# Kernel tuning notes

Measured on AMD Instinct MI355X. Metric: run time of the kernel, lower is better.

The kernel has to match this reference:

```python
import jax, jax.numpy as jnp
import numpy as np

N_NODES = 100000
BN_EPS = 1e-5


def gcn_conv(x, src, dst, W, b, n):
    # PyG GCNConv: add self-loops, symmetric norm D^-1/2 (A+I) D^-1/2, then linear.
    h = x @ W                                   # [N, F_out]
    deg = jnp.zeros((n,), h.dtype).at[dst].add(1.0)   # in-degree incl. self-loops
    dinv = jnp.where(deg > 0, jax.lax.rsqrt(deg), 0.0)
    norm = dinv[src] * dinv[dst]                # [E+N]
    msg = h[src] * norm[:, None]                # gather + scale, [E+N, F_out]
    out = jax.ops.segment_sum(msg, dst, num_segments=n)
    return out + b


def setup_inputs() -> dict:
    key = jax.random.key(0)
    ks = jax.random.split(key, 6)
    N, E, F_in, H, C = N_NODES, 1600000, 128, 64, 64
    x = jax.random.normal(ks[0], (N, F_in), dtype=jnp.float32)
    edge_index = jax.random.randint(ks[1], (2, E), 0, N, dtype=jnp.int64)
    W1 = jax.random.normal(ks[2], (F_in, H), dtype=jnp.float32) * (1.0 / np.sqrt(F_in))
    b1 = jnp.zeros((H,), jnp.float32)
    W2 = jax.random.normal(ks[3], (H, C), dtype=jnp.float32) * (1.0 / np.sqrt(H))
    b2 = jnp.zeros((C,), jnp.float32)
    gamma = jnp.ones((H,), jnp.float32)
    beta = jnp.zeros((H,), jnp.float32)
    return {"x": x, "edge_index": edge_index, "W1": W1, "b1": b1,
            "W2": W2, "b2": b2, "gamma": gamma, "beta": beta}


def reference(x, edge_index, W1, b1, W2, b2, gamma, beta):
    n = x.shape[0]
    loop = jnp.arange(n, dtype=edge_index.dtype)
    src = jnp.concatenate([edge_index[0], loop])
    dst = jnp.concatenate([edge_index[1], loop])
    # dropout(p=0.8) acts as identity in eval mode (deterministic baseline)
    h = gcn_conv(x, src, dst, W1, b1, n)
    # BatchNorm1d with batch statistics (biased var), as in training-mode math
    mean = jnp.mean(h, axis=0)
    var = jnp.mean(jnp.square(h - mean), axis=0)
    h = (h - mean) * jax.lax.rsqrt(var + BN_EPS) * gamma + beta
    h = jax.nn.relu(h)
    out = gcn_conv(h, src, dst, W2, b2, n)
    return out
```

## Files before the change

kernel.cpp:

```cpp
#include <hip/hip_runtime.h>

#define BN_EPS 1e-5f
#define SCAN_CHUNK 2048
#define EPB 16384
#define NBUCK 512
#define NBG 512

__device__ __forceinline__ float bf2f(unsigned short u) {
  return __uint_as_float(((unsigned)u) << 16);
}
__device__ __forceinline__ unsigned short f2bf(float f) {
  unsigned b = __float_as_uint(f);
  b += 0x7FFFu + ((b >> 16) & 1u);
  return (unsigned short)(b >> 16);
}

template<int K, bool FUSE_BN, bool SCALE>
__device__ __forceinline__ void gemm_persist(
    float* __restrict__ Ws, float* __restrict__ Xs, float* __restrict__ bn_s,
    int tile0, int stride, int nT,
    const float* __restrict__ X, const float* __restrict__ W,
    const float* __restrict__ dinv, const float* __restrict__ stats,
    const float* __restrict__ gamma, const float* __restrict__ beta,
    unsigned short* __restrict__ Y, int n, float inv_n) {
  constexpr int XS = K + 4;
  constexpr int RV = K / 4;
  constexpr int NL = (64 * RV) / 256;
  const int t = threadIdx.x;

  if (FUSE_BN) {
    if (t < 64) {
      float mean = stats[t] * inv_n;
      float var = stats[64 + t] * inv_n - mean * mean;
      bn_s[t] = mean;
      bn_s[64 + t] = rsqrtf(var + BN_EPS) * gamma[t];
      bn_s[128 + t] = beta[t];
    }
  }
  {
    const float4* wv = (const float4*)W;
    float4* wsv = (float4*)Ws;
    for (int idx = t; idx < K * 16; idx += 256) wsv[idx] = wv[idx];
  }

  const int tc = t & 15;
  const int tr = t >> 4;

  float4 xg[NL];
  int tile = tile0;
  {
    int base = tile * 64;
#pragma unroll
    for (int j = 0; j < NL; ++j) {
      int idx = t + j * 256;
      int row = idx / RV, kk = idx % RV;
      float4 v = make_float4(0.f, 0.f, 0.f, 0.f);
      if (base + row < n) v = *(const float4*)(X + (size_t)(base + row) * K + kk * 4);
      xg[j] = v;
    }
  }
  __syncthreads();
  {
    int base = tile * 64;
#pragma unroll
    for (int j = 0; j < NL; ++j) {
      int idx = t + j * 256;
      int row = idx / RV, kk = idx % RV;
      float4 v = xg[j];
      if (FUSE_BN && base + row < n) {
        int k0 = kk * 4;
        v.x = fmaxf(fmaf(v.x - bn_s[k0 + 0], bn_s[64 + k0 + 0], bn_s[128 + k0 + 0]), 0.f);
        v.y = fmaxf(fmaf(v.y - bn_s[k0 + 1], bn_s[64 + k0 + 1], bn_s[128 + k0 + 1]), 0.f);
        v.z = fmaxf(fmaf(v.z - bn_s[k0 + 2], bn_s[64 + k0 + 2], bn_s[128 + k0 + 2]), 0.f);
        v.w = fmaxf(fmaf(v.w - bn_s[k0 + 3], bn_s[64 + k0 + 3], bn_s[128 + k0 + 3]), 0.f);
      }
      *(float4*)(Xs + row * XS + kk * 4) = v;
    }
  }
  __syncthreads();

  for (;;) {
    const int next = tile + stride;
    const bool havenext = (next < nT);
    if (havenext) {
      int nb2 = next * 64;
#pragma unroll
      for (int j = 0; j < NL; ++j) {
        int idx = t + j * 256;
        int row = idx / RV, kk = idx % RV;
        float4 v = make_float4(0.f, 0.f, 0.f, 0.f);
        if (nb2 + row < n) v = *(const float4*)(X + (size_t)(nb2 + row) * K + kk * 4);
        xg[j] = v;
      }
    }

    float acc[4][4];
#pragma unroll
    for (int r = 0; r < 4; ++r)
#pragma unroll
      for (int c = 0; c < 4; ++c) acc[r][c] = 0.f;

#pragma unroll 4
    for (int k = 0; k < K; k += 4) {
      float4 xr[4], wr[4];
#pragma unroll
      for (int r = 0; r < 4; ++r) xr[r] = *(const float4*)(Xs + (tr * 4 + r) * XS + k);
#pragma unroll
      for (int kk = 0; kk < 4; ++kk) wr[kk] = *(const float4*)(Ws + (k + kk) * 64 + tc * 4);
#pragma unroll
      for (int kk = 0; kk < 4; ++kk) {
#pragma unroll
        for (int r = 0; r < 4; ++r) {
          float xv = (kk == 0) ? xr[r].x : (kk == 1) ? xr[r].y : (kk == 2) ? xr[r].z : xr[r].w;
          acc[r][0] = fmaf(xv, wr[kk].x, acc[r][0]);
          acc[r][1] = fmaf(xv, wr[kk].y, acc[r][1]);
          acc[r][2] = fmaf(xv, wr[kk].z, acc[r][2]);
          acc[r][3] = fmaf(xv, wr[kk].w, acc[r][3]);
        }
      }
    }

    {
      int base = tile * 64;
#pragma unroll
      for (int r = 0; r < 4; ++r) {
        int i = base + tr * 4 + r;
        if (i < n) {
          float sc = SCALE ? dinv[i] : 1.0f;
          ushort4 o;
          o.x = f2bf(acc[r][0] * sc);
          o.y = f2bf(acc[r][1] * sc);
          o.z = f2bf(acc[r][2] * sc);
          o.w = f2bf(acc[r][3] * sc);
          *(ushort4*)(Y + (size_t)i * 64 + tc * 4) = o;
        }
      }
    }

    if (!havenext) break;
    __syncthreads();
    {
      int nb2 = next * 64;
#pragma unroll
      for (int j = 0; j < NL; ++j) {
        int idx = t + j * 256;
        int row = idx / RV, kk = idx % RV;
        float4 v = xg[j];
        if (FUSE_BN && nb2 + row < n) {
          int k0 = kk * 4;
          v.x = fmaxf(fmaf(v.x - bn_s[k0 + 0], bn_s[64 + k0 + 0], bn_s[128 + k0 + 0]), 0.f);
          v.y = fmaxf(fmaf(v.y - bn_s[k0 + 1], bn_s[64 + k0 + 1], bn_s[128 + k0 + 1]), 0.f);
          v.z = fmaxf(fmaf(v.z - bn_s[k0 + 2], bn_s[64 + k0 + 2], bn_s[128 + k0 + 2]), 0.f);
          v.w = fmaxf(fmaf(v.w - bn_s[k0 + 3], bn_s[64 + k0 + 3], bn_s[128 + k0 + 3]), 0.f);
        }
        *(float4*)(Xs + row * XS + kk * 4) = v;
      }
    }
    __syncthreads();
    tile = next;
  }
}

__global__ __launch_bounds__(256) void k_fused_hist_gemm1(
    const int* __restrict__ dst, int* __restrict__ bh, int E, int nba,
    const float* __restrict__ X, const float* __restrict__ W,
    unsigned short* __restrict__ Y, int n, int nT) {
  __shared__ float Ws[128 * 64];
  __shared__ float Xs[64 * 132];

  if ((int)blockIdx.x < nba) {
    int* hist = (int*)Xs;
    const int t = threadIdx.x;
    const int idx = blockIdx.x;
    for (int b = t; b < NBUCK; b += 256) hist[b] = 0;
    __syncthreads();
    int ebase = idx * EPB;
#pragma unroll
    for (int i = 0; i < EPB / 1024; ++i) {
      int e = ebase + (i * 256 + t) * 4;
      if (e + 3 < E) {
        int4 d4 = *(const int4*)(dst + e);
        atomicAdd(&hist[d4.x >> 8], 1);
        atomicAdd(&hist[d4.y >> 8], 1);
        atomicAdd(&hist[d4.z >> 8], 1);
        atomicAdd(&hist[d4.w >> 8], 1);
      } else {
        for (int q = e; q < E && q < e + 4; ++q) atomicAdd(&hist[dst[q] >> 8], 1);
      }
    }
    __syncthreads();
    for (int b = t; b < NBUCK; b += 256) bh[(size_t)b * nba + idx] = hist[b];
    return;
  }
  int pid = blockIdx.x - nba;
  int stride = gridDim.x - nba;
  gemm_persist<128, false, false>(Ws, Xs, nullptr, pid, stride, nT,
                                  X, W, nullptr, nullptr, nullptr, nullptr,
                                  Y, n, 0.f);
}

__global__ __launch_bounds__(256) void k_bscan_local(int* __restrict__ a,
                                                     int* __restrict__ bsum, int M) {
  __shared__ int ts[256];
  int base = blockIdx.x * SCAN_CHUNK;
  int t = threadIdx.x;
  int idx0 = base + t * 8;
  int v[8];
  int s = 0;
#pragma unroll
  for (int k = 0; k < 8; ++k) {
    int i = idx0 + k;
    int d = (i < M) ? a[i] : 0;
    v[k] = s;
    s += d;
  }
  int val = s;
  ts[t] = val;
  __syncthreads();
#pragma unroll
  for (int off = 1; off < 256; off <<= 1) {
    int add = (t >= off) ? ts[t - off] : 0;
    __syncthreads();
    val += add;
    ts[t] = val;
    __syncthreads();
  }
  int excl = val - s;
#pragma unroll
  for (int k = 0; k < 8; ++k) {
    int i = idx0 + k;
    if (i < M) a[i] = excl + v[k];
  }
  if (t == 255) bsum[blockIdx.x] = val;
}

__global__ void k_bscan_blk(int* __restrict__ bsum, int nblk) {
  if (threadIdx.x == 0) {
    int run = 0;
    for (int i = 0; i < nblk; ++i) { int v = bsum[i]; bsum[i] = run; run += v; }
  }
}

__global__ __launch_bounds__(256) void k_bscan_add(int* __restrict__ a,
                                                   const int* __restrict__ bsum, int M) {
  int off = bsum[blockIdx.x];
  int base = blockIdx.x * SCAN_CHUNK;
  for (int k = threadIdx.x; k < SCAN_CHUNK; k += 256) {
    int i = base + k;
    if (i < M) a[i] += off;
  }
}

__global__ __launch_bounds__(256) void k_scatter(
    const int* __restrict__ src, const int* __restrict__ dst,
    const int* __restrict__ bh, int* __restrict__ sval, int E, int nba) {
  __shared__ int cur[NBUCK];
  const int t = threadIdx.x;
  for (int b = t; b < NBUCK; b += 256) cur[b] = bh[(size_t)b * nba + blockIdx.x];
  __syncthreads();
  int ebase = blockIdx.x * EPB;
#pragma unroll
  for (int i = 0; i < EPB / 1024; ++i) {
    int e = ebase + (i * 256 + t) * 4;
    if (e + 3 < E) {
      int4 d4 = *(const int4*)(dst + e);
      int4 s4 = *(const int4*)(src + e);
      int p0 = atomicAdd(&cur[d4.x >> 8], 1);
      int p1 = atomicAdd(&cur[d4.y >> 8], 1);
      int p2 = atomicAdd(&cur[d4.z >> 8], 1);
      int p3 = atomicAdd(&cur[d4.w >> 8], 1);
      sval[p0] = s4.x | ((d4.x & 255) << 20);
      sval[p1] = s4.y | ((d4.y & 255) << 20);
      sval[p2] = s4.z | ((d4.z & 255) << 20);
      sval[p3] = s4.w | ((d4.w & 255) << 20);
    } else {
      for (int q = e; q < E && q < e + 4; ++q) {
        int d = dst[q];
        int p = atomicAdd(&cur[d >> 8], 1);
        sval[p] = src[q] | ((d & 255) << 20);
      }
    }
  }
}

__global__ __launch_bounds__(256) void k_group_deg(
    const int* __restrict__ sval, const int* __restrict__ bh,
    int* __restrict__ deg, int nba, int n) {
  __shared__ int cnt[256];
  const int t = threadIdx.x;
  const int b = blockIdx.x;
  cnt[t] = 0;
  __syncthreads();
  int lo = bh[(size_t)b * nba];
  int end = bh[(size_t)(b + 1) * nba];
  for (int i = lo + t; i < end; i += 256)
    atomicAdd(&cnt[(sval[i] >> 20) & 255], 1);
  __syncthreads();
  int node = b * 256 + t;
  if (node < n) deg[node] = cnt[t];
}


__global__ __launch_bounds__(256) void k_scan_local(const int* __restrict__ deg,
                                                    int* __restrict__ row_ptr,
                                                    int* __restrict__ blksum,
                                                    float* __restrict__ dinv, int n) {
  __shared__ int ts[256];
  int base = blockIdx.x * SCAN_CHUNK;
  int t = threadIdx.x;
  int idx0 = base + t * 8;
  int v[8];
  int s = 0;
#pragma unroll
  for (int k = 0; k < 8; ++k) {
    int i = idx0 + k;
    int d = (i < n) ? deg[i] : 0;
    if (i < n) dinv[i] = rsqrtf(1.0f + (float)d);
    v[k] = s;
    s += d;
  }
  int val = s;
  ts[t] = val;
  __syncthreads();
#pragma unroll
  for (int off = 1; off < 256; off <<= 1) {
    int add = (t >= off) ? ts[t - off] : 0;
    __syncthreads();
    val += add;
    ts[t] = val;
    __syncthreads();
  }
  int excl = val - s;
#pragma unroll
  for (int k = 0; k < 8; ++k) {
    int i = idx0 + k;
    if (i < n) row_ptr[i] = excl + v[k];
  }
  if (t == 255) blksum[blockIdx.x] = val;
}

__global__ void k_scan_blk(int* __restrict__ blksum, int nblk,
                           int* __restrict__ row_ptr, int n,
                           float* __restrict__ stats) {
  for (int i = threadIdx.x; i < 128; i += 64) stats[i] = 0.f;
  if (threadIdx.x == 0) {
    int run = 0;
    for (int i = 0; i < nblk; ++i) { int v = blksum[i]; blksum[i] = run; run += v; }
    row_ptr[n] = run;
  }
}

__global__ __launch_bounds__(256) void k_scan_add(int* __restrict__ row_ptr,
                                                  const int* __restrict__ blksum, int n) {
  int off = blksum[blockIdx.x];
  int base = blockIdx.x * SCAN_CHUNK;
  for (int k = threadIdx.x; k < SCAN_CHUNK; k += 256) {
    int i = base + k;
    if (i < n) row_ptr[i] += off;
  }
}

__global__ __launch_bounds__(256) void k_fused_fill_scale(
    const int* __restrict__ sval, const int* __restrict__ bh,
    const int* __restrict__ row_ptr, int* __restrict__ col, int nba, int nbu,
    unsigned short* __restrict__ h16, const float* __restrict__ dinv, int n) {
  __shared__ int cur[256];
  const int t = threadIdx.x;
  if ((int)blockIdx.x < nbu) {
    const int b = blockIdx.x;
    int node = b * 256 + t;
    cur[t] = (node < n) ? row_ptr[node] : 0;
    __syncthreads();
    int lo = bh[(size_t)b * nba];
    int end = bh[(size_t)(b + 1) * nba];
    for (int i = lo + t; i < end; i += 256) {
      int v = sval[i];
      int p = atomicAdd(&cur[(v >> 20) & 255], 1);
      col[p] = v & 0x1FFFF;
    }
    return;
  }
  int si = blockIdx.x - nbu;
  int idx = (si * 256 + t) * 8;
  if (idx >= n * 64) return;
  int row = idx >> 6;
  float di = dinv[row];
  uint4 v = *(const uint4*)(h16 + idx);
  unsigned r[4] = {v.x, v.y, v.z, v.w};
#pragma unroll
  for (int q = 0; q < 4; ++q) {
    float lo = bf2f((unsigned short)(r[q] & 0xFFFFu)) * di;
    float hi = bf2f((unsigned short)(r[q] >> 16)) * di;
    r[q] = ((unsigned)f2bf(hi) << 16) | f2bf(lo);
  }
  *(uint4*)(h16 + idx) = make_uint4(r[0], r[1], r[2], r[3]);
}

__global__ __launch_bounds__(256) void k_gather_p(
    const unsigned short* __restrict__ Hs,
    const int* __restrict__ row_ptr,
    const int* __restrict__ col,
    const float* __restrict__ dinv,
    const float* __restrict__ b,
    float* __restrict__ out, int n) {
  const uint2* H64 = (const uint2*)Hs;
  int lane = threadIdx.x & 63;
  int wv = threadIdx.x >> 6;
  int i = blockIdx.x * 4 + wv;
  if (i >= n) return;
  int quarter = lane >> 4;
  int q = lane & 15;
  int p0 = row_ptr[i], p1 = row_ptr[i + 1];
  int nl = p1 - p0;
  int L = nl + 1;
  int cl = (lane == 0) ? i : ((lane <= nl) ? col[p0 + lane - 1] : i);
  int Lc = (L < 32) ? L : 32;
  bool two = (Lc > 16);

  uint2 u[8];
  float ww[8];
#pragma unroll
  for (int s = 0; s < 4; ++s) {
    int vidx = quarter * 4 + s;
    int vc = (vidx < Lc) ? vidx : 0;
    int c = __shfl(cl, vc);
    u[s] = H64[(size_t)c * 16 + q];
    ww[s] = (vidx < Lc) ? 1.0f : 0.0f;
  }
  if (two) {
#pragma unroll
    for (int s = 4; s < 8; ++s) {
      int vidx = 16 + quarter * 4 + (s - 4);
      int vc = (vidx < Lc) ? vidx : 0;
      int c = __shfl(cl, vc);
      u[s] = H64[(size_t)c * 16 + q];
      ww[s] = (vidx < Lc) ? 1.0f : 0.0f;
    }
  }

  float a0 = 0.f, a1 = 0.f, a2 = 0.f, a3 = 0.f;
#pragma unroll
  for (int s = 0; s < 4; ++s) {
    a0 = fmaf(ww[s], bf2f((unsigned short)u[s].x), a0);
    a1 = fmaf(ww[s], bf2f((unsigned short)(u[s].x >> 16)), a1);
    a2 = fmaf(ww[s], bf2f((unsigned short)u[s].y), a2);
    a3 = fmaf(ww[s], bf2f((unsigned short)(u[s].y >> 16)), a3);
  }
  if (two) {
#pragma unroll
    for (int s = 4; s < 8; ++s) {
      a0 = fmaf(ww[s], bf2f((unsigned short)u[s].x), a0);
      a1 = fmaf(ww[s], bf2f((unsigned short)(u[s].x >> 16)), a1);
      a2 = fmaf(ww[s], bf2f((unsigned short)u[s].y), a2);
      a3 = fmaf(ww[s], bf2f((unsigned short)(u[s].y >> 16)), a3);
    }
  }
  for (int v = 32 + quarter; v < L; v += 4) {
    int c = col[p0 + v - 1];
    uint2 uu = H64[(size_t)c * 16 + q];
    a0 += bf2f((unsigned short)uu.x);
    a1 += bf2f((unsigned short)(uu.x >> 16));
    a2 += bf2f((unsigned short)uu.y);
    a3 += bf2f((unsigned short)(uu.y >> 16));
  }
  a0 += __shfl_down(a0, 16); a0 += __shfl_down(a0, 32);
  a1 += __shfl_down(a1, 16); a1 += __shfl_down(a1, 32);
  a2 += __shfl_down(a2, 16); a2 += __shfl_down(a2, 32);
  a3 += __shfl_down(a3, 16); a3 += __shfl_down(a3, 32);
  if (lane < 16) {
    float di = dinv[i];
    float4 bb = *(const float4*)(b + 4 * q);
    float4 o;
    o.x = fmaf(di, a0, bb.x);
    o.y = fmaf(di, a1, bb.y);
    o.z = fmaf(di, a2, bb.z);
    o.w = fmaf(di, a3, bb.w);
    *(float4*)(out + (size_t)i * 64 + 4 * q) = o;
  }
}

__global__ __launch_bounds__(256) void k_bnstats(const float* __restrict__ A,
                                                 float* __restrict__ stats, int n) {
  int j = threadIdx.x & 63;
  int r = threadIdx.x >> 6;
  float s = 0.f, s2 = 0.f;
  for (int i = blockIdx.x * 4 + r; i < n; i += gridDim.x * 4) {
    float v = A[(size_t)i * 64 + j];
    s += v;
    s2 += v * v;
  }
  __shared__ float ls[256], ls2[256];
  ls[threadIdx.x] = s;
  ls2[threadIdx.x] = s2;
  __syncthreads();
  if (threadIdx.x < 64) {
    atomicAdd(&stats[j], ls[j] + ls[j + 64] + ls[j + 128] + ls[j + 192]);
    atomicAdd(&stats[64 + j], ls2[j] + ls2[j + 64] + ls2[j + 128] + ls2[j + 192]);
  }
}

__global__ __launch_bounds__(256) void k_gemm2(const float* __restrict__ X,
                                               const float* __restrict__ W,
                                               const float* __restrict__ dinv,
                                               const float* __restrict__ stats,
                                               const float* __restrict__ gamma,
                                               const float* __restrict__ beta,
                                               unsigned short* __restrict__ Y,
                                               int n, float inv_n, int nT) {
  __shared__ float Ws[64 * 64];
  __shared__ float Xs[64 * 68];
  __shared__ float bn_s[192];
  gemm_persist<64, true, true>(Ws, Xs, bn_s, blockIdx.x, gridDim.x, nT,
                               X, W, dinv, stats, gamma, beta, Y, n, inv_n);
}


extern "C" void kernel_launch(void* const* d_in, const int* in_sizes, int n_in,
                              void* d_out, int out_size, void* d_ws, size_t ws_size,
                              hipStream_t stream) {
  const float* x     = (const float*)d_in[0];
  const int*   ei    = (const int*)d_in[1];
  const float* W1    = (const float*)d_in[2];
  const float* b1    = (const float*)d_in[3];
  const float* W2    = (const float*)d_in[4];
  const float* b2    = (const float*)d_in[5];
  const float* gamma = (const float*)d_in[6];
  const float* beta  = (const float*)d_in[7];
  float* out = (float*)d_out;

  const int N = in_sizes[0] / 128;
  const int E = in_sizes[1] / 2;
  const int* src = ei;
  const int* dst = ei + E;

  const size_t Npad = ((size_t)N + 256) & ~(size_t)255;

  char* p = (char*)d_ws;
  float* dinv    = (float*)p;               p += Npad * 4;
  int*   deg     = (int*)p;                 p += Npad * 4;
  int*   row_ptr = (int*)p;                 p += Npad * 4;
  int*   blksum  = (int*)p;                 p += 256 * 4;
  int*   sval    = (int*)p;                 p += (size_t)E * 4;
  int*   col     = (int*)p;                 p += (size_t)E * 4;
  unsigned short* h16 = (unsigned short*)p; p += (size_t)N * 64 * 2;
  float* agg     = (float*)p;               p += (size_t)N * 64 * 4;
  float* stats   = (float*)p;               p += 128 * 4;

  int* bh = (int*)agg;

  int nb_n4 = (N + 3) / 4;
  int nb_t  = (N + 63) / 64;
  int nba   = (E + EPB - 1) / EPB;
  int nbu   = (N + 255) / 256;
  int nbS   = (N * 64 + 2047) / 2048;
  int nscan = (N + SCAN_CHUNK - 1) / SCAN_CHUNK;
  int M     = NBUCK * nba;
  int nbM   = (M + SCAN_CHUNK - 1) / SCAN_CHUNK;
  float inv_n = 1.0f / (float)N;

  k_fused_hist_gemm1<<<nba + NBG, 256, 0, stream>>>(dst, bh, E, nba,
                                                    x, W1, h16, N, nb_t);

  k_bscan_local<<<nbM, 256, 0, stream>>>(bh, blksum, M);
  k_bscan_blk<<<1, 64, 0, stream>>>(blksum, nbM);
  k_bscan_add<<<nbM, 256, 0, stream>>>(bh, blksum, M);
  k_scatter<<<nba, 256, 0, stream>>>(src, dst, bh, sval, E, nba);

  k_group_deg<<<nbu, 256, 0, stream>>>(sval, bh, deg, nba, N);

  k_scan_local<<<nscan, 256, 0, stream>>>(deg, row_ptr, blksum, dinv, N);
  k_scan_blk<<<1, 64, 0, stream>>>(blksum, nscan, row_ptr, N, stats);
  k_scan_add<<<nscan, 256, 0, stream>>>(row_ptr, blksum, N);

  k_fused_fill_scale<<<nbu + nbS, 256, 0, stream>>>(sval, bh, row_ptr, col,
                                                    nba, nbu, h16, dinv, N);

  k_gather_p<<<nb_n4, 256, 0, stream>>>(h16, row_ptr, col, dinv, b1, agg, N);

  k_bnstats<<<1024, 256, 0, stream>>>(agg, stats, N);

  k_gemm2<<<NBG, 256, 0, stream>>>(agg, W2, dinv, stats, gamma, beta, h16, N,
                                   inv_n, nb_t);
  k_gather_p<<<nb_n4, 256, 0, stream>>>(h16, row_ptr, col, dinv, b2, out, N);
}
```

Before: 327.4 us.

## Fuse scan block-sum passes and degree histogram into fewer kernel launches

Drops the single-threaded block-sum scan kernels. Each add-kernel block now reduces the preceding block sums from shared memory itself. The per-bucket degree count is merged with the local prefix scan into one kernel that handles eight buckets per block, and the scatter kernel moves to 512 threads so one block covers all 512 bucket cursors. This cuts the launch count and serial tiny kernels. In exchange each block does redundant serial prefix work, and the shared-memory scans assume at most 64 blocks.

```diff
diff --git a/kernel.cpp b/kernel.cpp
--- a/kernel.cpp
+++ b/kernel.cpp
@@ -234,34 +234,39 @@
   if (t == 255) bsum[blockIdx.x] = val;
 }
 
-__global__ void k_bscan_blk(int* __restrict__ bsum, int nblk) {
-  if (threadIdx.x == 0) {
+__global__ __launch_bounds__(256) void k_bscan_add2(int* __restrict__ a,
+                                                    const int* __restrict__ bsum,
+                                                    int M, int nblk) {
+  __shared__ int ls[64];
+  __shared__ int soff;
+  const int t = threadIdx.x;
+  if (t < nblk) ls[t] = bsum[t];
+  __syncthreads();
+  if (t == 0) {
     int run = 0;
-    for (int i = 0; i < nblk; ++i) { int v = bsum[i]; bsum[i] = run; run += v; }
-  }
-}
-
-__global__ __launch_bounds__(256) void k_bscan_add(int* __restrict__ a,
-                                                   const int* __restrict__ bsum, int M) {
-  int off = bsum[blockIdx.x];
+    for (int i = 0; i < (int)blockIdx.x; ++i) run += ls[i];
+    soff = run;
+  }
+  __syncthreads();
+  int off = soff;
   int base = blockIdx.x * SCAN_CHUNK;
-  for (int k = threadIdx.x; k < SCAN_CHUNK; k += 256) {
+  for (int k = t; k < SCAN_CHUNK; k += 256) {
     int i = base + k;
     if (i < M) a[i] += off;
   }
 }
 
-__global__ __launch_bounds__(256) void k_scatter(
+__global__ __launch_bounds__(512) void k_scatter(
     const int* __restrict__ src, const int* __restrict__ dst,
     const int* __restrict__ bh, int* __restrict__ sval, int E, int nba) {
   __shared__ int cur[NBUCK];
   const int t = threadIdx.x;
-  for (int b = t; b < NBUCK; b += 256) cur[b] = bh[(size_t)b * nba + blockIdx.x];
+  if (t < NBUCK) cur[t] = bh[(size_t)t * nba + blockIdx.x];
   __syncthreads();
   int ebase = blockIdx.x * EPB;
 #pragma unroll
-  for (int i = 0; i < EPB / 1024; ++i) {
-    int e = ebase + (i * 256 + t) * 4;
+  for (int i = 0; i < EPB / 2048; ++i) {
+    int e = ebase + (i * 512 + t) * 4;
     if (e + 3 < E) {
       int4 d4 = *(const int4*)(dst + e);
       int4 s4 = *(const int4*)(src + e);
@@ -283,38 +288,32 @@
   }
 }
 
-__global__ __launch_bounds__(256) void k_group_deg(
+__global__ __launch_bounds__(256) void k_deg_scan(
     const int* __restrict__ sval, const int* __restrict__ bh,
-    int* __restrict__ deg, int nba, int n) {
-  __shared__ int cnt[256];
+    int* __restrict__ row_ptr, int* __restrict__ blksum,
+    float* __restrict__ dinv, int nba, int n) {
+  __shared__ int cnt[2048];
+  __shared__ int ts[256];
   const int t = threadIdx.x;
-  const int b = blockIdx.x;
-  cnt[t] = 0;
-  __syncthreads();
-  int lo = bh[(size_t)b * nba];
-  int end = bh[(size_t)(b + 1) * nba];
-  for (int i = lo + t; i < end; i += 256)
-    atomicAdd(&cnt[(sval[i] >> 20) & 255], 1);
-  __syncthreads();
-  int node = b * 256 + t;
-  if (node < n) deg[node] = cnt[t];
-}
-
-
-__global__ __launch_bounds__(256) void k_scan_local(const int* __restrict__ deg,
-                                                    int* __restrict__ row_ptr,
-                                                    int* __restrict__ blksum,
-                                                    float* __restrict__ dinv, int n) {
-  __shared__ int ts[256];
+  for (int j = t; j < 2048; j += 256) cnt[j] = 0;
+  __syncthreads();
+#pragma unroll
+  for (int j = 0; j < 8; ++j) {
+    int bu = blockIdx.x * 8 + j;
+    int lo = bh[(size_t)bu * nba];
+    int end = bh[(size_t)(bu + 1) * nba];
+    for (int i = lo + t; i < end; i += 256)
+      atomicAdd(&cnt[j * 256 + ((sval[i] >> 20) & 255)], 1);
+  }
+  __syncthreads();
   int base = blockIdx.x * SCAN_CHUNK;
-  int t = threadIdx.x;
   int idx0 = base + t * 8;
   int v[8];
   int s = 0;
 #pragma unroll
   for (int k = 0; k < 8; ++k) {
     int i = idx0 + k;
-    int d = (i < n) ? deg[i] : 0;
+    int d = (i < n) ? cnt[t * 8 + k] : 0;
     if (i < n) dinv[i] = rsqrtf(1.0f + (float)d);
     v[k] = s;
     s += d;
@@ -339,22 +338,32 @@
   if (t == 255) blksum[blockIdx.x] = val;
 }
 
-__global__ void k_scan_blk(int* __restrict__ blksum, int nblk,
-                           int* __restrict__ row_ptr, int n,
-                           float* __restrict__ stats) {
-  for (int i = threadIdx.x; i < 128; i += 64) stats[i] = 0.f;
-  if (threadIdx.x == 0) {
+__global__ __launch_bounds__(256) void k_scan_add2(int* __restrict__ row_ptr,
+                                                   const int* __restrict__ blksum,
+                                                   float* __restrict__ stats,
+                                                   int n, int nblk) {
+  __shared__ int ls[64];
+  __shared__ int soff;
+  const int t = threadIdx.x;
+  if (t < nblk) ls[t] = blksum[t];
+  __syncthreads();
+  if (t == 0) {
     int run = 0;
-    for (int i = 0; i < nblk; ++i) { int v = blksum[i]; blksum[i] = run; run += v; }
-    row_ptr[n] = run;
-  }
-}
-
-__global__ __launch_bounds__(256) void k_scan_add(int* __restrict__ row_ptr,
-                                                  const int* __restrict__ blksum, int n) {
-  int off = blksum[blockIdx.x];
+    for (int i = 0; i < (int)blockIdx.x; ++i) run += ls[i];
+    soff = run;
+  }
+  __syncthreads();
+  int off = soff;
+  if (blockIdx.x == 0) {
+    if (t < 128) stats[t] = 0.f;
+    if (t == 0) {
+      int tot = 0;
+      for (int i = 0; i < nblk; ++i) tot += ls[i];
+      row_ptr[n] = tot;
+    }
+  }
   int base = blockIdx.x * SCAN_CHUNK;
-  for (int k = threadIdx.x; k < SCAN_CHUNK; k += 256) {
+  for (int k = t; k < SCAN_CHUNK; k += 256) {
     int i = base + k;
     if (i < n) row_ptr[i] += off;
   }
@@ -537,7 +546,7 @@
 
   char* p = (char*)d_ws;
   float* dinv    = (float*)p;               p += Npad * 4;
-  int*   deg     = (int*)p;                 p += Npad * 4;
+  int*   unused  = (int*)p;                 p += Npad * 4;
   int*   row_ptr = (int*)p;                 p += Npad * 4;
   int*   blksum  = (int*)p;                 p += 256 * 4;
   int*   sval    = (int*)p;                 p += (size_t)E * 4;
@@ -545,6 +554,7 @@
   unsigned short* h16 = (unsigned short*)p; p += (size_t)N * 64 * 2;
   float* agg     = (float*)p;               p += (size_t)N * 64 * 4;
   float* stats   = (float*)p;               p += 128 * 4;
+  (void)unused;
 
   int* bh = (int*)agg;
 
@@ -562,15 +572,11 @@
                                                     x, W1, h16, N, nb_t);
 
   k_bscan_local<<<nbM, 256, 0, stream>>>(bh, blksum, M);
-  k_bscan_blk<<<1, 64, 0, stream>>>(blksum, nbM);
-  k_bscan_add<<<nbM, 256, 0, stream>>>(bh, blksum, M);
-  k_scatter<<<nba, 256, 0, stream>>>(src, dst, bh, sval, E, nba);
-
-  k_group_deg<<<nbu, 256, 0, stream>>>(sval, bh, deg, nba, N);
-
-  k_scan_local<<<nscan, 256, 0, stream>>>(deg, row_ptr, blksum, dinv, N);
-  k_scan_blk<<<1, 64, 0, stream>>>(blksum, nscan, row_ptr, N, stats);
-  k_scan_add<<<nscan, 256, 0, stream>>>(row_ptr, blksum, N);
+  k_bscan_add2<<<nbM, 256, 0, stream>>>(bh, blksum, M, nbM);
+  k_scatter<<<nba, 512, 0, stream>>>(src, dst, bh, sval, E, nba);
+
+  k_deg_scan<<<nscan, 256, 0, stream>>>(sval, bh, row_ptr, blksum, dinv, nba, N);
+  k_scan_add2<<<nscan, 256, 0, stream>>>(row_ptr, blksum, stats, N, nscan);
 
   k_fused_fill_scale<<<nbu + nbS, 256, 0, stream>>>(sval, bh, row_ptr, col,
                                                     nba, nbu, h16, dinv, N);
```

After: 332.7 us. Within noise of the previous version (+1.6%).
